# Performance work log

Measured on AMD Instinct MI355X. Metric: run time of the kernel, lower is better.

Reference implementation:

```python
import jax, jax.numpy as jnp
import numpy as np


def setup_inputs() -> dict:
    key = jax.random.key(0)
    k1, k2, k3, k4 = jax.random.split(key, 4)
    B, H, L, D = 2, 16, 2048, 64
    q = jax.random.normal(k1, (B, H, L, D), dtype=jnp.float32)
    k = jax.random.normal(k2, (B, H, L, D), dtype=jnp.float32)
    v = jax.random.normal(k3, (B, H, L, D), dtype=jnp.float32)
    mask = jax.random.randint(k4, (B, 1, L, L), 0, 2, dtype=jnp.int32)
    return {"q": q, "k": k, "v": v, "mask": mask}


def reference(q, k, v, mask):
    d_tensor = q.shape[-1]
    # NegativeReLU: pass through only negative values and 0
    v_neg = -jax.nn.relu(-v)
    # score: [B,H,L,L]
    score = jnp.einsum("bhqd,bhkd->bhqk", q, k) / jnp.sqrt(
        jnp.asarray(d_tensor, dtype=q.dtype))
    score = jnp.where(mask == 0, jnp.asarray(-10000.0, dtype=score.dtype), score)
    attn = jax.nn.softmax(score, axis=-1)
    return jnp.einsum("bhqk,bhkd->bhqd", attn, v_neg)
```

## Files before the change

kernel.cpp:

```cpp
#include <hip/hip_runtime.h>
#include <math.h>

typedef __bf16 bf16_t;
typedef bf16_t bf16x8 __attribute__((ext_vector_type(8)));
typedef float  f32x16 __attribute__((ext_vector_type(16)));
typedef float  f32x4  __attribute__((ext_vector_type(4)));

#define MFMA32(a, b, c) __builtin_amdgcn_mfma_f32_32x32x16_bf16((a), (b), (c), 0, 0, 0)

static __device__ __forceinline__ unsigned pk_bf16(float a, float b) {
  union { bf16_t h[2]; unsigned u; } t;
  t.h[0] = (bf16_t)a;
  t.h[1] = (bf16_t)b;
  return t.u;
}

static __device__ __forceinline__ unsigned pk_trunc(float a, float b) {
  return (__float_as_uint(a) >> 16) | (__float_as_uint(b) & 0xFFFF0000u);
}

__global__ __launch_bounds__(256) void prepass(
    const float* __restrict__ kp, const float* __restrict__ vp,
    const int* __restrict__ maskp, bf16_t* __restrict__ kfr,
    bf16_t* __restrict__ vfr, unsigned long long* __restrict__ mpk) {
  const int sect = blockIdx.x >> 11;
  const int blk  = blockIdx.x & 2047;
  const int tid  = threadIdx.x;

  if (sect == 0) {
    const size_t t = (size_t)blk * 256 + tid;
    const int ln = t & 63, dc = (t >> 6) & 3;
    const int kh = (t >> 8) & 63, bh = (int)(t >> 14);
    const float* s = kp + ((size_t)(bh * 2048 + kh * 32 + (ln & 31))) * 64 +
                     dc * 16 + (ln >> 5) * 8;
    f32x4 a0 = *(const f32x4*)s;
    f32x4 a1 = *(const f32x4*)(s + 4);
    bf16x8 w;
#pragma unroll
    for (int j = 0; j < 4; ++j) { w[j] = (bf16_t)a0[j]; w[4 + j] = (bf16_t)a1[j]; }
    *(bf16x8*)(kfr + t * 8) = w;
  } else if (sect == 1) {
    const size_t t = (size_t)blk * 256 + tid;
    const int ln = t & 63, rr = (t >> 6) & 1, kc = (t >> 7) & 1;
    const int p = (t >> 8) & 1, kt = (t >> 9) & 31, bh = (int)(t >> 14);
    const int d   = rr * 32 + (ln & 31);
    const int key = kt * 64 + p * 32 + kc * 16 + (ln >> 5) * 8;
    const float* s = vp + ((size_t)(bh * 2048 + key)) * 64 + d;
    bf16_t w[8];
#pragma unroll
    for (int j = 0; j < 8; ++j) w[j] = (bf16_t)fminf(s[(size_t)j * 64], 0.f);
    *(bf16x8*)(vfr + t * 8) = *(bf16x8*)w;
  } else {
    const int lane = tid & 63;
    const int gw   = blk * 4 + (tid >> 6);
    const int bq   = gw >> 1, half = gw & 1;
    const int b    = bq >> 11, q = bq & 2047;
    const size_t base = (size_t)bq * 2048 + half * 1024;
    unsigned long long w = 0;
#pragma unroll
    for (int j = 0; j < 16; ++j) {
      const int mv = maskp[base + j * 64 + lane];
      const unsigned long long bal = __ballot(mv != 0);
      if (lane == j) w = bal;
    }
    if (lane < 16) mpk[((size_t)b * 32 + half * 16 + lane) * 2048 + q] = w;
  }
}

__global__ __launch_bounds__(256, 4) void nrev_attn_ws(
    const float* __restrict__ qp, const bf16_t* __restrict__ kfr,
    const bf16_t* __restrict__ vfr, const unsigned long long* __restrict__ mpk,
    float* __restrict__ outp) {
  constexpr int L = 2048, D = 64;
  __shared__ float Oe[2][64][68];
  __shared__ float lsum[2][2][32];

  const int tid  = threadIdx.x;
  const int lane = tid & 63;
  const int wv   = tid >> 6;
  const int p    = wv >> 1;
  const int g    = wv & 1;
  const int col  = lane & 31;
  const int hh   = lane >> 5;
  const int blk  = blockIdx.x;
  const int bh   = (blk & 7) * 4 + (blk >> 8);
  const int qt   = (blk >> 3) & 31;
  const int bb   = bh >> 4;
  const int q0   = qt * 64;
  const float c1 = 0.18033688011112042f;

  bf16x8 qf[4];
  {
    const float* gq = qp + (size_t)(bh * L + q0 + g * 32 + col) * D;
#pragma unroll
    for (int dc = 0; dc < 4; ++dc) {
      const float* ptr = gq + dc * 16 + hh * 8;
      f32x4 f0 = *(const f32x4*)ptr;
      f32x4 f1 = *(const f32x4*)(ptr + 4);
      bf16x8 t;
#pragma unroll
      for (int j = 0; j < 4; ++j) {
        t[j]     = (bf16_t)(f0[j] * c1);
        t[4 + j] = (bf16_t)(f1[j] * c1);
      }
      qf[dc] = t;
    }
  }

  const char* kpt = (const char*)kfr + (size_t)bh * 262144 + p * 4096 + (size_t)lane * 16;
  const char* vpt = (const char*)vfr + (size_t)bh * 262144 + p * 4096 + (size_t)lane * 16;
  const unsigned long long* mrow = mpk + (size_t)bb * 65536 + q0 + g * 32 + col;

  f32x16 acc0, acc1;
#pragma unroll
  for (int i = 0; i < 16; ++i) { acc0[i] = 0.f; acc1[i] = 0.f; }
  float l_run = 0.f;

  bf16x8 kf0 = *(const bf16x8*)(kpt + 0);
  bf16x8 kf1 = *(const bf16x8*)(kpt + 1024);
  bf16x8 kf2 = *(const bf16x8*)(kpt + 2048);
  bf16x8 kf3 = *(const bf16x8*)(kpt + 3072);
  unsigned long long bits = mrow[0];

  for (int it = 0; it < 32; ++it) {
    const int itn = (it < 31) ? it + 1 : 31;
    const char* kn = kpt + (size_t)itn * 8192;
    bf16x8 kn0 = *(const bf16x8*)(kn + 0);
    bf16x8 kn1 = *(const bf16x8*)(kn + 1024);
    bf16x8 kn2 = *(const bf16x8*)(kn + 2048);
    bf16x8 kn3 = *(const bf16x8*)(kn + 3072);
    const char* vg = vpt + (size_t)it * 8192;
    bf16x8 vf0 = *(const bf16x8*)(vg + 0);
    bf16x8 vf1 = *(const bf16x8*)(vg + 1024);
    bf16x8 vf2 = *(const bf16x8*)(vg + 2048);
    bf16x8 vf3 = *(const bf16x8*)(vg + 3072);
    const unsigned long long bits_n = mrow[(size_t)itn * 2048];

    f32x16 st0;
#pragma unroll
    for (int i = 0; i < 16; ++i) st0[i] = 0.f;
    st0 = MFMA32(kf0, qf[0], st0);
    st0 = MFMA32(kf1, qf[1], st0);
    st0 = MFMA32(kf2, qf[2], st0);
    st0 = MFMA32(kf3, qf[3], st0);

    const unsigned kb32 = ((unsigned)(bits >> (32 * p))) >> (4 * hh);
    float Sl = 0.f;
#pragma unroll
    for (int r = 0; r < 16; ++r) {
      const int c = (r & 3) + 8 * (r >> 2);
      float p0 = __builtin_amdgcn_exp2f(st0[r]);
      p0 = ((kb32 >> c) & 1u) ? p0 : 0.f;
      st0[r] = p0;
      Sl += p0;
    }
    Sl += __shfl_xor(Sl, 32);
    l_run += Sl;

#pragma unroll
    for (int kc = 0; kc < 2; ++kc) {
      const unsigned pk0  = pk_trunc(st0[8 * kc + 0], st0[8 * kc + 1]);
      const unsigned pk0b = pk_trunc(st0[8 * kc + 2], st0[8 * kc + 3]);
      const unsigned pk1  = pk_trunc(st0[8 * kc + 4], st0[8 * kc + 5]);
      const unsigned pk1b = pk_trunc(st0[8 * kc + 6], st0[8 * kc + 7]);
      const unsigned sh0  = __shfl_xor(pk0, 32);
      const unsigned sh0b = __shfl_xor(pk0b, 32);
      const unsigned sh1  = __shfl_xor(pk1, 32);
      const unsigned sh1b = __shfl_xor(pk1b, 32);
      union { unsigned u[4]; bf16x8 v; } bbv;
      bbv.u[0] = hh ? sh1  : pk0;
      bbv.u[1] = hh ? sh1b : pk0b;
      bbv.u[2] = hh ? pk1  : sh0;
      bbv.u[3] = hh ? pk1b : sh0b;
      if (kc == 0) {
        acc0 = MFMA32(vf0, bbv.v, acc0);
        acc1 = MFMA32(vf1, bbv.v, acc1);
      } else {
        acc0 = MFMA32(vf2, bbv.v, acc0);
        acc1 = MFMA32(vf3, bbv.v, acc1);
      }
    }

    kf0 = kn0; kf1 = kn1; kf2 = kn2; kf3 = kn3;
    bits = bits_n;
  }

  if (hh == 0) lsum[g][p][col] = l_run;
  __syncthreads();
  const float scale = 1.f / (lsum[g][0][col] + lsum[g][1][col]);

#pragma unroll
  for (int dt = 0; dt < 2; ++dt) {
#pragma unroll
    for (int g2 = 0; g2 < 4; ++g2) {
      f32x4 w;
#pragma unroll
      for (int j = 0; j < 4; ++j)
        w[j] = (dt ? acc1[g2 * 4 + j] : acc0[g2 * 4 + j]) * scale;
      *(f32x4*)&Oe[p][g * 32 + col][g2 * 8 + hh * 4 + dt * 32] = w;
    }
  }
  __syncthreads();
#pragma unroll
  for (int i = 0; i < 4; ++i) {
    const int idx = tid + i * 256;
    const int row = idx >> 4, c4 = idx & 15;
    f32x4 v0 = *(const f32x4*)&Oe[0][row][c4 * 4];
    f32x4 v1 = *(const f32x4*)&Oe[1][row][c4 * 4];
    f32x4 vs = v0 + v1;
    *(f32x4*)&outp[(size_t)(bh * L + q0 + row) * D + c4 * 4] = vs;
  }
}

__global__ __launch_bounds__(256, 4) void nrev_attn_fb(
    const float* __restrict__ qp, const float* __restrict__ kp,
    const float* __restrict__ vp, const int* __restrict__ maskp,
    float* __restrict__ outp) {
  constexpr int L = 2048, D = 64;
  __shared__ union alignas(16) SMem {
    struct {
      bf16_t K[64 * 72];
      bf16_t V[64 * 72];
      unsigned long long mb[64];
    } s;
    float Oe[2][64][68];
  } sm;
  __shared__ float mlbuf[2][2][32][2];

  const int tid  = threadIdx.x;
  const int lane = tid & 63;
  const int wv   = tid >> 6;
  const int p    = wv >> 1;
  const int g    = wv & 1;
  const int col  = lane & 31;
  const int hh   = lane >> 5;
  const int blk  = blockIdx.x;
  const int bh   = (blk & 7) * 4 + (blk >> 8);
  const int qt   = (blk >> 3) & 31;
  const int bb   = bh >> 4;
  const int q0   = qt * 64;
  const float c1 = 0.18033688011112042f;

  bf16x8 qf[4];
  {
    const float* gq = qp + (size_t)(bh * L + q0 + g * 32 + col) * D;
#pragma unroll
    for (int dc = 0; dc < 4; ++dc) {
      const float* ptr = gq + dc * 16 + hh * 8;
      f32x4 f0 = *(const f32x4*)ptr;
      f32x4 f1 = *(const f32x4*)(ptr + 4);
      bf16x8 t;
#pragma unroll
      for (int j = 0; j < 4; ++j) {
        t[j]     = (bf16_t)(f0[j] * c1);
        t[4 + j] = (bf16_t)(f1[j] * c1);
      }
      qf[dc] = t;
    }
  }

  f32x16 acc0, acc1;
#pragma unroll
  for (int i = 0; i < 16; ++i) { acc0[i] = 0.f; acc1[i] = 0.f; }
  float m_run = -__builtin_inff();
  float l_run = 0.f;

  for (int kt = 0; kt < L; kt += 64) {
    __syncthreads();
    {
      const int key = tid >> 2, dp = tid & 3;
      const float* gk = kp + (size_t)(bh * L + kt + key) * D + dp * 16;
      f32x4 a0 = *(const f32x4*)gk;
      f32x4 a1 = *(const f32x4*)(gk + 4);
      f32x4 a2 = *(const f32x4*)(gk + 8);
      f32x4 a3 = *(const f32x4*)(gk + 12);
      bf16x8 w0, w1;
#pragma unroll
      for (int j = 0; j < 4; ++j) {
        w0[j] = (bf16_t)a0[j]; w0[4 + j] = (bf16_t)a1[j];
        w1[j] = (bf16_t)a2[j]; w1[4 + j] = (bf16_t)a3[j];
      }
      *(bf16x8*)&sm.s.K[key * 72 + dp * 16]     = w0;
      *(bf16x8*)&sm.s.K[key * 72 + dp * 16 + 8] = w1;
    }
    {
      const int w16 = wv * 16;
      const float* gv = vp + (size_t)(bh * L + kt + w16) * D + lane;
      bf16x8 w0, w1;
#pragma unroll
      for (int i = 0; i < 8; ++i) {
        w0[i] = (bf16_t)fminf(gv[(size_t)i * D], 0.f);
        w1[i] = (bf16_t)fminf(gv[(size_t)(i + 8) * D], 0.f);
      }
      *(bf16x8*)&sm.s.V[lane * 72 + w16]     = w0;
      *(bf16x8*)&sm.s.V[lane * 72 + w16 + 8] = w1;
    }
    for (int i = 0; i < 16; ++i) {
      const int row = wv * 16 + i;
      int mv = maskp[(size_t)bb * L * L + (size_t)(q0 + row) * L + kt + lane];
      unsigned long long bal = __ballot(mv != 0);
      if (lane == 0) sm.s.mb[row] = bal;
    }
    __syncthreads();

    f32x16 st0;
#pragma unroll
    for (int i = 0; i < 16; ++i) st0[i] = 0.f;
#pragma unroll
    for (int dc = 0; dc < 4; ++dc) {
      bf16x8 a0 = *(const bf16x8*)&sm.s.K[(p * 32 + col) * 72 + dc * 16 + hh * 8];
      st0 = MFMA32(a0, qf[dc], st0);
    }

    float M = st0[0];
#pragma unroll
    for (int r = 1; r < 16; ++r) M = fmaxf(M, st0[r]);
#pragma unroll
    for (int sh = 1; sh < 64; sh <<= 1) M = fmaxf(M, __shfl_xor(M, sh));
    if (M > m_run) {
      const float alpha = exp2f(m_run - M);
      l_run *= alpha;
#pragma unroll
      for (int r = 0; r < 16; ++r) { acc0[r] *= alpha; acc1[r] *= alpha; }
      m_run = M;
    }

    const unsigned long long bits = sm.s.mb[g * 32 + col];
    const unsigned kb = ((unsigned)(bits >> (32 * p))) >> (4 * hh);
    float Sl = 0.f;
#pragma unroll
    for (int r = 0; r < 16; ++r) {
      const int c = (r & 3) + 8 * (r >> 2);
      float p0 = exp2f(st0[r] - m_run);
      p0 = ((kb >> c) & 1u) ? p0 : 0.f;
      st0[r] = p0;
      Sl += p0;
    }
    Sl += __shfl_xor(Sl, 32);
    l_run += Sl;

#pragma unroll
    for (int kc = 0; kc < 2; ++kc) {
      const unsigned pk0  = pk_bf16(st0[8 * kc + 0], st0[8 * kc + 1]);
      const unsigned pk0b = pk_bf16(st0[8 * kc + 2], st0[8 * kc + 3]);
      const unsigned pk1  = pk_bf16(st0[8 * kc + 4], st0[8 * kc + 5]);
      const unsigned pk1b = pk_bf16(st0[8 * kc + 6], st0[8 * kc + 7]);
      const unsigned sh0  = __shfl_xor(pk0, 32);
      const unsigned sh0b = __shfl_xor(pk0b, 32);
      const unsigned sh1  = __shfl_xor(pk1, 32);
      const unsigned sh1b = __shfl_xor(pk1b, 32);
      union { unsigned u[4]; bf16x8 v; } bbv;
      bbv.u[0] = hh ? sh1  : pk0;
      bbv.u[1] = hh ? sh1b : pk0b;
      bbv.u[2] = hh ? pk1  : sh0;
      bbv.u[3] = hh ? pk1b : sh0b;
      const int kbase = p * 32 + kc * 16 + hh * 8;
      bf16x8 av0 = *(const bf16x8*)&sm.s.V[col * 72        + kbase];
      bf16x8 av1 = *(const bf16x8*)&sm.s.V[(col + 32) * 72 + kbase];
      acc0 = MFMA32(av0, bbv.v, acc0);
      acc1 = MFMA32(av1, bbv.v, acc1);
    }
  }

  if (hh == 0) {
    mlbuf[g][p][col][0] = m_run;
    mlbuf[g][p][col][1] = l_run;
  }
  __syncthreads();
  const float m0 = mlbuf[g][0][col][0], l0v = mlbuf[g][0][col][1];
  const float m1 = mlbuf[g][1][col][0], l1v = mlbuf[g][1][col][1];
  const float ms = fmaxf(m0, m1);
  const float a0s = exp2f(m0 - ms), a1s = exp2f(m1 - ms);
  const float lst = a0s * l0v + a1s * l1v;
  const float scale = (p ? a1s : a0s) / lst;

#pragma unroll
  for (int dt = 0; dt < 2; ++dt) {
#pragma unroll
    for (int g2 = 0; g2 < 4; ++g2) {
      f32x4 w;
#pragma unroll
      for (int j = 0; j < 4; ++j)
        w[j] = (dt ? acc1[g2 * 4 + j] : acc0[g2 * 4 + j]) * scale;
      *(f32x4*)&sm.Oe[p][g * 32 + col][g2 * 8 + hh * 4 + dt * 32] = w;
    }
  }
  __syncthreads();
#pragma unroll
  for (int i = 0; i < 4; ++i) {
    const int idx = tid + i * 256;
    const int row = idx >> 4, c4 = idx & 15;
    f32x4 v0 = *(const f32x4*)&sm.Oe[0][row][c4 * 4];
    f32x4 v1 = *(const f32x4*)&sm.Oe[1][row][c4 * 4];
    f32x4 vs = v0 + v1;
    *(f32x4*)&outp[(size_t)(bh * L + q0 + row) * D + c4 * 4] = vs;
  }
}

extern "C" void kernel_launch(void* const* d_in, const int* in_sizes, int n_in,
                              void* d_out, int out_size, void* d_ws, size_t ws_size,
                              hipStream_t stream) {
  (void)in_sizes; (void)n_in; (void)out_size;
  const float* qp = (const float*)d_in[0];
  const float* kp = (const float*)d_in[1];
  const float* vp = (const float*)d_in[2];
  const int*   mp = (const int*)d_in[3];
  float* op = (float*)d_out;

  const size_t kOff = 0;
  const size_t vOff = (size_t)8 * 1024 * 1024;
  const size_t mOff = (size_t)16 * 1024 * 1024;
  const size_t need = mOff + (size_t)1024 * 1024;

  if (d_ws != nullptr && ws_size >= need) {
    bf16_t* kb = (bf16_t*)((char*)d_ws + kOff);
    bf16_t* vt = (bf16_t*)((char*)d_ws + vOff);
    unsigned long long* mpk = (unsigned long long*)((char*)d_ws + mOff);
    hipLaunchKernelGGL(prepass, dim3(6144), dim3(256), 0, stream,
                       kp, vp, mp, kb, vt, mpk);
    hipLaunchKernelGGL(nrev_attn_ws, dim3(1024), dim3(256), 0, stream,
                       qp, kb, vt, mpk, op);
  } else {
    hipLaunchKernelGGL(nrev_attn_fb, dim3(1024), dim3(256), 0, stream,
                       qp, kp, vp, mp, op);
  }
}
```

Baseline: 164.9 us.

## Process two 32-row query tiles per wave to reuse K/V fragments

New measurement: 197.1 us. 19.5% more time.

```diff
diff --git a/kernel.cpp b/kernel.cpp
--- a/kernel.cpp
+++ b/kernel.cpp
@@ -67,13 +67,13 @@
   }
 }
 
-__global__ __launch_bounds__(256, 4) void nrev_attn_ws(
+__global__ __launch_bounds__(256, 2) void nrev_attn_ws(
     const float* __restrict__ qp, const bf16_t* __restrict__ kfr,
     const bf16_t* __restrict__ vfr, const unsigned long long* __restrict__ mpk,
     float* __restrict__ outp) {
   constexpr int L = 2048, D = 64;
-  __shared__ float Oe[2][64][68];
-  __shared__ float lsum[2][2][32];
+  __shared__ float Oe[128][68];
+  __shared__ float lsum[2][2][2][32];
 
   const int tid  = threadIdx.x;
   const int lane = tid & 63;
@@ -83,15 +83,16 @@
   const int col  = lane & 31;
   const int hh   = lane >> 5;
   const int blk  = blockIdx.x;
-  const int bh   = (blk & 7) * 4 + (blk >> 8);
-  const int qt   = (blk >> 3) & 31;
+  const int bh   = (blk & 7) * 4 + (blk >> 7);
+  const int qt   = (blk >> 3) & 15;
   const int bb   = bh >> 4;
-  const int q0   = qt * 64;
+  const int q0   = qt * 128;
   const float c1 = 0.18033688011112042f;
 
-  bf16x8 qf[4];
-  {
-    const float* gq = qp + (size_t)(bh * L + q0 + g * 32 + col) * D;
+  bf16x8 qfA[4], qfB[4];
+#pragma unroll
+  for (int n = 0; n < 2; ++n) {
+    const float* gq = qp + (size_t)(bh * L + q0 + g * 64 + n * 32 + col) * D;
 #pragma unroll
     for (int dc = 0; dc < 4; ++dc) {
       const float* ptr = gq + dc * 16 + hh * 8;
@@ -103,24 +104,26 @@
         t[j]     = (bf16_t)(f0[j] * c1);
         t[4 + j] = (bf16_t)(f1[j] * c1);
       }
-      qf[dc] = t;
+      if (n == 0) qfA[dc] = t; else qfB[dc] = t;
     }
   }
 
   const char* kpt = (const char*)kfr + (size_t)bh * 262144 + p * 4096 + (size_t)lane * 16;
   const char* vpt = (const char*)vfr + (size_t)bh * 262144 + p * 4096 + (size_t)lane * 16;
-  const unsigned long long* mrow = mpk + (size_t)bb * 65536 + q0 + g * 32 + col;
-
-  f32x16 acc0, acc1;
-#pragma unroll
-  for (int i = 0; i < 16; ++i) { acc0[i] = 0.f; acc1[i] = 0.f; }
-  float l_run = 0.f;
+  const unsigned long long* mrowA = mpk + (size_t)bb * 65536 + q0 + g * 64 + col;
+  const unsigned long long* mrowB = mrowA + 32;
+
+  f32x16 accA0, accA1, accB0, accB1;
+#pragma unroll
+  for (int i = 0; i < 16; ++i) { accA0[i] = 0.f; accA1[i] = 0.f; accB0[i] = 0.f; accB1[i] = 0.f; }
+  float lA = 0.f, lB = 0.f;
 
   bf16x8 kf0 = *(const bf16x8*)(kpt + 0);
   bf16x8 kf1 = *(const bf16x8*)(kpt + 1024);
   bf16x8 kf2 = *(const bf16x8*)(kpt + 2048);
   bf16x8 kf3 = *(const bf16x8*)(kpt + 3072);
-  unsigned long long bits = mrow[0];
+  unsigned long long bitsA = mrowA[0];
+  unsigned long long bitsB = mrowB[0];
 
   for (int it = 0; it < 32; ++it) {
     const int itn = (it < 31) ? it + 1 : 31;
@@ -134,81 +137,122 @@
     bf16x8 vf1 = *(const bf16x8*)(vg + 1024);
     bf16x8 vf2 = *(const bf16x8*)(vg + 2048);
     bf16x8 vf3 = *(const bf16x8*)(vg + 3072);
-    const unsigned long long bits_n = mrow[(size_t)itn * 2048];
-
-    f32x16 st0;
-#pragma unroll
-    for (int i = 0; i < 16; ++i) st0[i] = 0.f;
-    st0 = MFMA32(kf0, qf[0], st0);
-    st0 = MFMA32(kf1, qf[1], st0);
-    st0 = MFMA32(kf2, qf[2], st0);
-    st0 = MFMA32(kf3, qf[3], st0);
-
-    const unsigned kb32 = ((unsigned)(bits >> (32 * p))) >> (4 * hh);
-    float Sl = 0.f;
+    const unsigned long long bAn = mrowA[(size_t)itn * 2048];
+    const unsigned long long bBn = mrowB[(size_t)itn * 2048];
+
+    f32x16 stA, stB;
+#pragma unroll
+    for (int i = 0; i < 16; ++i) { stA[i] = 0.f; stB[i] = 0.f; }
+    stA = MFMA32(kf0, qfA[0], stA);  stB = MFMA32(kf0, qfB[0], stB);
+    stA = MFMA32(kf1, qfA[1], stA);  stB = MFMA32(kf1, qfB[1], stB);
+    stA = MFMA32(kf2, qfA[2], stA);  stB = MFMA32(kf2, qfB[2], stB);
+    stA = MFMA32(kf3, qfA[3], stA);  stB = MFMA32(kf3, qfB[3], stB);
+
+    const unsigned kbA = ((unsigned)(bitsA >> (32 * p))) >> (4 * hh);
+    const unsigned kbB = ((unsigned)(bitsB >> (32 * p))) >> (4 * hh);
+    float SlA = 0.f, SlB = 0.f;
 #pragma unroll
     for (int r = 0; r < 16; ++r) {
       const int c = (r & 3) + 8 * (r >> 2);
-      float p0 = __builtin_amdgcn_exp2f(st0[r]);
-      p0 = ((kb32 >> c) & 1u) ? p0 : 0.f;
-      st0[r] = p0;
-      Sl += p0;
-    }
-    Sl += __shfl_xor(Sl, 32);
-    l_run += Sl;
+      float pa = __builtin_amdgcn_exp2f(stA[r]);
+      float pb = __builtin_amdgcn_exp2f(stB[r]);
+      pa = ((kbA >> c) & 1u) ? pa : 0.f;
+      pb = ((kbB >> c) & 1u) ? pb : 0.f;
+      stA[r] = pa; stB[r] = pb;
+      SlA += pa; SlB += pb;
+    }
+    SlA += __shfl_xor(SlA, 32);
+    SlB += __shfl_xor(SlB, 32);
+    lA += SlA; lB += SlB;
 
 #pragma unroll
     for (int kc = 0; kc < 2; ++kc) {
-      const unsigned pk0  = pk_trunc(st0[8 * kc + 0], st0[8 * kc + 1]);
-      const unsigned pk0b = pk_trunc(st0[8 * kc + 2], st0[8 * kc + 3]);
-      const unsigned pk1  = pk_trunc(st0[8 * kc + 4], st0[8 * kc + 5]);
-      const unsigned pk1b = pk_trunc(st0[8 * kc + 6], st0[8 * kc + 7]);
-      const unsigned sh0  = __shfl_xor(pk0, 32);
-      const unsigned sh0b = __shfl_xor(pk0b, 32);
-      const unsigned sh1  = __shfl_xor(pk1, 32);
-      const unsigned sh1b = __shfl_xor(pk1b, 32);
-      union { unsigned u[4]; bf16x8 v; } bbv;
-      bbv.u[0] = hh ? sh1  : pk0;
-      bbv.u[1] = hh ? sh1b : pk0b;
-      bbv.u[2] = hh ? pk1  : sh0;
-      bbv.u[3] = hh ? pk1b : sh0b;
-      if (kc == 0) {
-        acc0 = MFMA32(vf0, bbv.v, acc0);
-        acc1 = MFMA32(vf1, bbv.v, acc1);
-      } else {
-        acc0 = MFMA32(vf2, bbv.v, acc0);
-        acc1 = MFMA32(vf3, bbv.v, acc1);
+#pragma unroll
+      for (int n = 0; n < 2; ++n) {
+        const f32x16& st = n ? stB : stA;
+        const unsigned pk0  = pk_trunc(st[8 * kc + 0], st[8 * kc + 1]);
+        const unsigned pk0b = pk_trunc(st[8 * kc + 2], st[8 * kc + 3]);
+        const unsigned pk1  = pk_trunc(st[8 * kc + 4], st[8 * kc + 5]);
+        const unsigned pk1b = pk_trunc(st[8 * kc + 6], st[8 * kc + 7]);
+        const unsigned sh0  = __shfl_xor(pk0, 32);
+        const unsigned sh0b = __shfl_xor(pk0b, 32);
+        const unsigned sh1  = __shfl_xor(pk1, 32);
+        const unsigned sh1b = __shfl_xor(pk1b, 32);
+        union { unsigned u[4]; bf16x8 v; } bbv;
+        bbv.u[0] = hh ? sh1  : pk0;
+        bbv.u[1] = hh ? sh1b : pk0b;
+        bbv.u[2] = hh ? pk1  : sh0;
+        bbv.u[3] = hh ? pk1b : sh0b;
+        if (n == 0) {
+          accA0 = MFMA32(kc ? vf2 : vf0, bbv.v, accA0);
+          accA1 = MFMA32(kc ? vf3 : vf1, bbv.v, accA1);
+        } else {
+          accB0 = MFMA32(kc ? vf2 : vf0, bbv.v, accB0);
+          accB1 = MFMA32(kc ? vf3 : vf1, bbv.v, accB1);
+        }
       }
     }
 
     kf0 = kn0; kf1 = kn1; kf2 = kn2; kf3 = kn3;
-    bits = bits_n;
-  }
-
-  if (hh == 0) lsum[g][p][col] = l_run;
+    bitsA = bAn; bitsB = bBn;
+  }
+
+  if (hh == 0) {
+    lsum[g][0][p][col] = lA;
+    lsum[g][1][p][col] = lB;
+  }
   __syncthreads();
-  const float scale = 1.f / (lsum[g][0][col] + lsum[g][1][col]);
-
-#pragma unroll
-  for (int dt = 0; dt < 2; ++dt) {
-#pragma unroll
-    for (int g2 = 0; g2 < 4; ++g2) {
-      f32x4 w;
-#pragma unroll
-      for (int j = 0; j < 4; ++j)
-        w[j] = (dt ? acc1[g2 * 4 + j] : acc0[g2 * 4 + j]) * scale;
-      *(f32x4*)&Oe[p][g * 32 + col][g2 * 8 + hh * 4 + dt * 32] = w;
+  const float scA = 1.f / (lsum[g][0][0][col] + lsum[g][0][1][col]);
+  const float scB = 1.f / (lsum[g][1][0][col] + lsum[g][1][1][col]);
+
+#pragma unroll
+  for (int n = 0; n < 2; ++n) {
+    const float sc = n ? scB : scA;
+    const int qrow = g * 64 + n * 32 + col;
+    if (p == 0) {
+#pragma unroll
+      for (int dt = 0; dt < 2; ++dt)
+#pragma unroll
+        for (int g2 = 0; g2 < 4; ++g2) {
+          f32x4 w;
+#pragma unroll
+          for (int j = 0; j < 4; ++j) {
+            const float a = n ? (dt ? accB1[g2 * 4 + j] : accB0[g2 * 4 + j])
+                              : (dt ? accA1[g2 * 4 + j] : accA0[g2 * 4 + j]);
+            w[j] = a * sc;
+          }
+          *(f32x4*)&Oe[qrow][g2 * 8 + hh * 4 + dt * 32] = w;
+        }
     }
   }
   __syncthreads();
 #pragma unroll
-  for (int i = 0; i < 4; ++i) {
+  for (int n = 0; n < 2; ++n) {
+    const float sc = n ? scB : scA;
+    const int qrow = g * 64 + n * 32 + col;
+    if (p == 1) {
+#pragma unroll
+      for (int dt = 0; dt < 2; ++dt)
+#pragma unroll
+        for (int g2 = 0; g2 < 4; ++g2) {
+          f32x4 w = *(f32x4*)&Oe[qrow][g2 * 8 + hh * 4 + dt * 32];
+#pragma unroll
+          for (int j = 0; j < 4; ++j) {
+            const float a = n ? (dt ? accB1[g2 * 4 + j] : accB0[g2 * 4 + j])
+                              : (dt ? accA1[g2 * 4 + j] : accA0[g2 * 4 + j]);
+            w[j] += a * sc;
+          }
+          *(f32x4*)&Oe[qrow][g2 * 8 + hh * 4 + dt * 32] = w;
+        }
+    }
+  }
+  __syncthreads();
+#pragma unroll
+  for (int i = 0; i < 8; ++i) {
     const int idx = tid + i * 256;
     const int row = idx >> 4, c4 = idx & 15;
-    f32x4 v0 = *(const f32x4*)&Oe[0][row][c4 * 4];
-    f32x4 v1 = *(const f32x4*)&Oe[1][row][c4 * 4];
-    f32x4 vs = v0 + v1;
-    *(f32x4*)&outp[(size_t)(bh * L + q0 + row) * D + c4 * 4] = vs;
+    f32x4 val = *(const f32x4*)&Oe[row][c4 * 4];
+    *(f32x4*)&outp[(size_t)(bh * L + q0 + row) * D + c4 * 4] = val;
   }
 }
 
@@ -418,7 +462,7 @@
     unsigned long long* mpk = (unsigned long long*)((char*)d_ws + mOff);
     hipLaunchKernelGGL(prepass, dim3(6144), dim3(256), 0, stream,
                        kp, vp, mp, kb, vt, mpk);
-    hipLaunchKernelGGL(nrev_attn_ws, dim3(1024), dim3(256), 0, stream,
+    hipLaunchKernelGGL(nrev_attn_ws, dim3(512), dim3(256), 0, stream,
                        qp, kb, vt, mpk, op);
   } else {
     hipLaunchKernelGGL(nrev_attn_fb, dim3(1024), dim3(256), 0, stream,
```

## Split key range across two blocks and add a combine kernel

Applied to the files above, without the earlier changes.

After: 180.7 us. 9.6% more time.

```diff
diff --git a/kernel.cpp b/kernel.cpp
--- a/kernel.cpp
+++ b/kernel.cpp
@@ -67,12 +67,12 @@
   }
 }
 
-__global__ __launch_bounds__(256, 4) void nrev_attn_ws(
+__global__ __launch_bounds__(256, 4) void nrev_attn_split(
     const float* __restrict__ qp, const bf16_t* __restrict__ kfr,
     const bf16_t* __restrict__ vfr, const unsigned long long* __restrict__ mpk,
-    float* __restrict__ outp) {
+    float* __restrict__ opart, float* __restrict__ lpart) {
   constexpr int L = 2048, D = 64;
-  __shared__ float Oe[2][64][68];
+  __shared__ float Oe[64][68];
   __shared__ float lsum[2][2][32];
 
   const int tid  = threadIdx.x;
@@ -83,10 +83,12 @@
   const int col  = lane & 31;
   const int hh   = lane >> 5;
   const int blk  = blockIdx.x;
-  const int bh   = (blk & 7) * 4 + (blk >> 8);
-  const int qt   = (blk >> 3) & 31;
+  const int bh   = (blk & 7) * 4 + (blk >> 9);
+  const int z    = (blk >> 3) & 1;
+  const int qt   = (blk >> 4) & 31;
   const int bb   = bh >> 4;
   const int q0   = qt * 64;
+  const int it0  = z * 16;
   const float c1 = 0.18033688011112042f;
 
   bf16x8 qf[4];
@@ -116,25 +118,19 @@
   for (int i = 0; i < 16; ++i) { acc0[i] = 0.f; acc1[i] = 0.f; }
   float l_run = 0.f;
 
-  bf16x8 kf0 = *(const bf16x8*)(kpt + 0);
-  bf16x8 kf1 = *(const bf16x8*)(kpt + 1024);
-  bf16x8 kf2 = *(const bf16x8*)(kpt + 2048);
-  bf16x8 kf3 = *(const bf16x8*)(kpt + 3072);
-  unsigned long long bits = mrow[0];
-
-  for (int it = 0; it < 32; ++it) {
-    const int itn = (it < 31) ? it + 1 : 31;
-    const char* kn = kpt + (size_t)itn * 8192;
-    bf16x8 kn0 = *(const bf16x8*)(kn + 0);
-    bf16x8 kn1 = *(const bf16x8*)(kn + 1024);
-    bf16x8 kn2 = *(const bf16x8*)(kn + 2048);
-    bf16x8 kn3 = *(const bf16x8*)(kn + 3072);
+  bf16x8 kf0 = *(const bf16x8*)(kpt + (size_t)it0 * 8192 + 0);
+  bf16x8 kf1 = *(const bf16x8*)(kpt + (size_t)it0 * 8192 + 1024);
+  bf16x8 kf2 = *(const bf16x8*)(kpt + (size_t)it0 * 8192 + 2048);
+  bf16x8 kf3 = *(const bf16x8*)(kpt + (size_t)it0 * 8192 + 3072);
+  unsigned long long bits = mrow[(size_t)it0 * 2048];
+
+  for (int it = it0; it < it0 + 16; ++it) {
     const char* vg = vpt + (size_t)it * 8192;
     bf16x8 vf0 = *(const bf16x8*)(vg + 0);
     bf16x8 vf1 = *(const bf16x8*)(vg + 1024);
     bf16x8 vf2 = *(const bf16x8*)(vg + 2048);
     bf16x8 vf3 = *(const bf16x8*)(vg + 3072);
-    const unsigned long long bits_n = mrow[(size_t)itn * 2048];
+    const unsigned long long bits_n = mrow[(size_t)(it + 1) * 2048];
 
     f32x16 st0;
 #pragma unroll
@@ -143,6 +139,12 @@
     st0 = MFMA32(kf1, qf[1], st0);
     st0 = MFMA32(kf2, qf[2], st0);
     st0 = MFMA32(kf3, qf[3], st0);
+
+    const char* kn = kpt + (size_t)(it + 1) * 8192;
+    kf0 = *(const bf16x8*)(kn + 0);
+    kf1 = *(const bf16x8*)(kn + 1024);
+    kf2 = *(const bf16x8*)(kn + 2048);
+    kf3 = *(const bf16x8*)(kn + 3072);
 
     const unsigned kb32 = ((unsigned)(bits >> (32 * p))) >> (4 * hh);
     float Sl = 0.f;
@@ -180,7 +182,174 @@
         acc1 = MFMA32(vf3, bbv.v, acc1);
       }
     }
-
+    bits = bits_n;
+  }
+
+  if (hh == 0) lsum[g][p][col] = l_run;
+  if (p == 0) {
+#pragma unroll
+    for (int dt = 0; dt < 2; ++dt)
+#pragma unroll
+      for (int g2 = 0; g2 < 4; ++g2) {
+        f32x4 w;
+#pragma unroll
+        for (int j = 0; j < 4; ++j)
+          w[j] = dt ? acc1[g2 * 4 + j] : acc0[g2 * 4 + j];
+        *(f32x4*)&Oe[g * 32 + col][g2 * 8 + hh * 4 + dt * 32] = w;
+      }
+  }
+  __syncthreads();
+  if (p == 1) {
+#pragma unroll
+    for (int dt = 0; dt < 2; ++dt)
+#pragma unroll
+      for (int g2 = 0; g2 < 4; ++g2) {
+        f32x4 w = *(f32x4*)&Oe[g * 32 + col][g2 * 8 + hh * 4 + dt * 32];
+#pragma unroll
+        for (int j = 0; j < 4; ++j)
+          w[j] += dt ? acc1[g2 * 4 + j] : acc0[g2 * 4 + j];
+        *(f32x4*)&Oe[g * 32 + col][g2 * 8 + hh * 4 + dt * 32] = w;
+      }
+  }
+  __syncthreads();
+  float* ob = opart + (((size_t)(z * 32 + bh) * 2048 + q0)) * 64;
+#pragma unroll
+  for (int i = 0; i < 4; ++i) {
+    const int idx = tid + i * 256;
+    const int row = idx >> 4, c4 = idx & 15;
+    *(f32x4*)&ob[(size_t)row * 64 + c4 * 4] = *(const f32x4*)&Oe[row][c4 * 4];
+  }
+  if (tid < 64) {
+    const float lt = lsum[tid >> 5][0][tid & 31] + lsum[tid >> 5][1][tid & 31];
+    lpart[(size_t)(z * 32 + bh) * 2048 + q0 + tid] = lt;
+  }
+}
+
+__global__ __launch_bounds__(256) void combine(
+    const float* __restrict__ opart, const float* __restrict__ lpart,
+    float* __restrict__ outp) {
+  const size_t idx = (size_t)blockIdx.x * 256 + threadIdx.x;
+  const size_t q   = idx >> 4;
+  f32x4 a = ((const f32x4*)opart)[idx];
+  f32x4 b = ((const f32x4*)(opart + (size_t)4194304))[idx];
+  const float l = lpart[q] + lpart[65536 + q];
+  f32x4 r = (a + b) * (1.f / l);
+  ((f32x4*)outp)[idx] = r;
+}
+
+__global__ __launch_bounds__(256, 2) void nrev_attn_ws4(
+    const float* __restrict__ qp, const bf16_t* __restrict__ kfr,
+    const bf16_t* __restrict__ vfr, const unsigned long long* __restrict__ mpk,
+    float* __restrict__ outp) {
+  constexpr int L = 2048, D = 64;
+  __shared__ float Oe[2][64][68];
+  __shared__ float lsum[2][2][32];
+
+  const int tid  = threadIdx.x;
+  const int lane = tid & 63;
+  const int wv   = tid >> 6;
+  const int p    = wv >> 1;
+  const int g    = wv & 1;
+  const int col  = lane & 31;
+  const int hh   = lane >> 5;
+  const int blk  = blockIdx.x;
+  const int bh   = (blk & 7) * 4 + (blk >> 8);
+  const int qt   = (blk >> 3) & 31;
+  const int bb   = bh >> 4;
+  const int q0   = qt * 64;
+  const float c1 = 0.18033688011112042f;
+
+  bf16x8 qf[4];
+  {
+    const float* gq = qp + (size_t)(bh * L + q0 + g * 32 + col) * D;
+#pragma unroll
+    for (int dc = 0; dc < 4; ++dc) {
+      const float* ptr = gq + dc * 16 + hh * 8;
+      f32x4 f0 = *(const f32x4*)ptr;
+      f32x4 f1 = *(const f32x4*)(ptr + 4);
+      bf16x8 t;
+#pragma unroll
+      for (int j = 0; j < 4; ++j) {
+        t[j]     = (bf16_t)(f0[j] * c1);
+        t[4 + j] = (bf16_t)(f1[j] * c1);
+      }
+      qf[dc] = t;
+    }
+  }
+
+  const char* kpt = (const char*)kfr + (size_t)bh * 262144 + p * 4096 + (size_t)lane * 16;
+  const char* vpt = (const char*)vfr + (size_t)bh * 262144 + p * 4096 + (size_t)lane * 16;
+  const unsigned long long* mrow = mpk + (size_t)bb * 65536 + q0 + g * 32 + col;
+
+  f32x16 acc0, acc1;
+#pragma unroll
+  for (int i = 0; i < 16; ++i) { acc0[i] = 0.f; acc1[i] = 0.f; }
+  float l_run = 0.f;
+
+  bf16x8 kf0 = *(const bf16x8*)(kpt + 0);
+  bf16x8 kf1 = *(const bf16x8*)(kpt + 1024);
+  bf16x8 kf2 = *(const bf16x8*)(kpt + 2048);
+  bf16x8 kf3 = *(const bf16x8*)(kpt + 3072);
+  unsigned long long bits = mrow[0];
+
+  for (int it = 0; it < 32; ++it) {
+    const int itn = (it < 31) ? it + 1 : 31;
+    const char* kn = kpt + (size_t)itn * 8192;
+    bf16x8 kn0 = *(const bf16x8*)(kn + 0);
+    bf16x8 kn1 = *(const bf16x8*)(kn + 1024);
+    bf16x8 kn2 = *(const bf16x8*)(kn + 2048);
+    bf16x8 kn3 = *(const bf16x8*)(kn + 3072);
+    const char* vg = vpt + (size_t)it * 8192;
+    bf16x8 vf0 = *(const bf16x8*)(vg + 0);
+    bf16x8 vf1 = *(const bf16x8*)(vg + 1024);
+    bf16x8 vf2 = *(const bf16x8*)(vg + 2048);
+    bf16x8 vf3 = *(const bf16x8*)(vg + 3072);
+    const unsigned long long bits_n = mrow[(size_t)itn * 2048];
+
+    f32x16 st0;
+#pragma unroll
+    for (int i = 0; i < 16; ++i) st0[i] = 0.f;
+    st0 = MFMA32(kf0, qf[0], st0);
+    st0 = MFMA32(kf1, qf[1], st0);
+    st0 = MFMA32(kf2, qf[2], st0);
+    st0 = MFMA32(kf3, qf[3], st0);
+
+    const unsigned kb32 = ((unsigned)(bits >> (32 * p))) >> (4 * hh);
+    float Sl = 0.f;
+#pragma unroll
+    for (int r = 0; r < 16; ++r) {
+      const int c = (r & 3) + 8 * (r >> 2);
+      float p0 = __builtin_amdgcn_exp2f(st0[r]);
+      p0 = ((kb32 >> c) & 1u) ? p0 : 0.f;
+      st0[r] = p0;
+      Sl += p0;
+    }
+    Sl += __shfl_xor(Sl, 32);
+    l_run += Sl;
+
+#pragma unroll
+    for (int kc = 0; kc < 2; ++kc) {
+      const unsigned pk0  = pk_trunc(st0[8 * kc + 0], st0[8 * kc + 1]);
+      const unsigned pk0b = pk_trunc(st0[8 * kc + 2], st0[8 * kc + 3]);
+      const unsigned pk1  = pk_trunc(st0[8 * kc + 4], st0[8 * kc + 5]);
+      const unsigned pk1b = pk_trunc(st0[8 * kc + 6], st0[8 * kc + 7]);
+      const unsigned sh0  = __shfl_xor(pk0, 32);
+      const unsigned sh0b = __shfl_xor(pk0b, 32);
+      const unsigned sh1  = __shfl_xor(pk1, 32);
+      const unsigned sh1b = __shfl_xor(pk1b, 32);
+      union { unsigned u[4]; bf16x8 v; } bbv;
+      bbv.u[0] = hh ? sh1  : pk0;
+      bbv.u[1] = hh ? sh1b : pk0b;
+      bbv.u[2] = hh ? pk1  : sh0;
+      bbv.u[3] = hh ? pk1b : sh0b;
+      if (kc == 0) {
+        acc0 = MFMA32(vf0, bbv.v, acc0);
+        acc1 = MFMA32(vf1, bbv.v, acc1);
+      } else {
+        acc0 = MFMA32(vf2, bbv.v, acc0);
+        acc1 = MFMA32(vf3, bbv.v, acc1);
+      }
+    }
     kf0 = kn0; kf1 = kn1; kf2 = kn2; kf3 = kn3;
     bits = bits_n;
   }
@@ -190,7 +359,7 @@
   const float scale = 1.f / (lsum[g][0][col] + lsum[g][1][col]);
 
 #pragma unroll
-  for (int dt = 0; dt < 2; ++dt) {
+  for (int dt = 0; dt < 2; ++dt)
 #pragma unroll
     for (int g2 = 0; g2 < 4; ++g2) {
       f32x4 w;
@@ -199,7 +368,6 @@
         w[j] = (dt ? acc1[g2 * 4 + j] : acc0[g2 * 4 + j]) * scale;
       *(f32x4*)&Oe[p][g * 32 + col][g2 * 8 + hh * 4 + dt * 32] = w;
     }
-  }
   __syncthreads();
 #pragma unroll
   for (int i = 0; i < 4; ++i) {
@@ -375,7 +543,7 @@
   const float scale = (p ? a1s : a0s) / lst;
 
 #pragma unroll
-  for (int dt = 0; dt < 2; ++dt) {
+  for (int dt = 0; dt < 2; ++dt)
 #pragma unroll
     for (int g2 = 0; g2 < 4; ++g2) {
       f32x4 w;
@@ -384,7 +552,6 @@
         w[j] = (dt ? acc1[g2 * 4 + j] : acc0[g2 * 4 + j]) * scale;
       *(f32x4*)&sm.Oe[p][g * 32 + col][g2 * 8 + hh * 4 + dt * 32] = w;
     }
-  }
   __syncthreads();
 #pragma unroll
   for (int i = 0; i < 4; ++i) {
@@ -410,15 +577,30 @@
   const size_t kOff = 0;
   const size_t vOff = (size_t)8 * 1024 * 1024;
   const size_t mOff = (size_t)16 * 1024 * 1024;
-  const size_t need = mOff + (size_t)1024 * 1024;
-
-  if (d_ws != nullptr && ws_size >= need) {
+  const size_t oOff = (size_t)17 * 1024 * 1024;
+  const size_t lOff = (size_t)49 * 1024 * 1024;
+  const size_t needFull = lOff + (size_t)512 * 1024;
+  const size_t needT2   = mOff + (size_t)1024 * 1024;
+
+  if (d_ws != nullptr && ws_size >= needFull) {
+    bf16_t* kb = (bf16_t*)((char*)d_ws + kOff);
+    bf16_t* vt = (bf16_t*)((char*)d_ws + vOff);
+    unsigned long long* mpk = (unsigned long long*)((char*)d_ws + mOff);
+    float* opart = (float*)((char*)d_ws + oOff);
+    float* lpart = (float*)((char*)d_ws + lOff);
+    hipLaunchKernelGGL(prepass, dim3(6144), dim3(256), 0, stream,
+                       kp, vp, mp, kb, vt, mpk);
+    hipLaunchKernelGGL(nrev_attn_split, dim3(2048), dim3(256), 0, stream,
+                       qp, kb, vt, mpk, opart, lpart);
+    hipLaunchKernelGGL(combine, dim3(4096), dim3(256), 0, stream,
+                       opart, lpart, op);
+  } else if (d_ws != nullptr && ws_size >= needT2) {
     bf16_t* kb = (bf16_t*)((char*)d_ws + kOff);
     bf16_t* vt = (bf16_t*)((char*)d_ws + vOff);
     unsigned long long* mpk = (unsigned long long*)((char*)d_ws + mOff);
     hipLaunchKernelGGL(prepass, dim3(6144), dim3(256), 0, stream,
                        kp, vp, mp, kb, vt, mpk);
-    hipLaunchKernelGGL(nrev_attn_ws, dim3(1024), dim3(256), 0, stream,
+    hipLaunchKernelGGL(nrev_attn_ws4, dim3(1024), dim3(256), 0, stream,
                        qp, kb, vt, mpk, op);
   } else {
     hipLaunchKernelGGL(nrev_attn_fb, dim3(1024), dim3(256), 0, stream,
```
